# Performance work log

Hardware: AMD Instinct MI355X
Metric: run time of the kernel (lower is better)

## Reference

```python
import jax, jax.numpy as jnp
import numpy as np

B, T, E, D, H, DK, DV, C, FILT = 32, 2048, 1024, 1024, 4, 512, 512, 10, 100
K = 2 * FILT + 1  # conv kernel width = 201
SCALING = 2.0     # default forward scaling arg


def setup_inputs() -> dict:
    key = jax.random.key(0)
    ks = jax.random.split(key, 12)
    s = 0.02
    enc_hs_pad = jax.random.normal(ks[0], (B, T, E), dtype=jnp.float32)
    enc_hs_len = jax.random.randint(ks[1], (B,), T // 2, T + 1).astype(jnp.int32)
    dec_z = jax.random.normal(ks[2], (B, D), dtype=jnp.float32)
    # default att_prev in the module: uniform over valid frames (per head)
    valid = (jnp.arange(T)[None, :] < enc_hs_len[:, None]).astype(jnp.float32)  # (B,T)
    att_prev = jnp.broadcast_to((valid / enc_hs_len[:, None].astype(jnp.float32))[:, None, :], (B, H, T))
    return {
        "enc_hs_pad": enc_hs_pad,
        "enc_hs_len": enc_hs_len,
        "dec_z": dec_z,
        "att_prev": att_prev,
        "Wq": s * jax.random.normal(ks[3], (H, D, DK), dtype=jnp.float32),
        "bq": s * jax.random.normal(ks[4], (H, DK), dtype=jnp.float32),
        "Wk": s * jax.random.normal(ks[5], (H, E, DK), dtype=jnp.float32),
        "Wv": s * jax.random.normal(ks[6], (H, E, DV), dtype=jnp.float32),
        "gw": s * jax.random.normal(ks[7], (H, DK), dtype=jnp.float32),
        "gb": s * jax.random.normal(ks[8], (H,), dtype=jnp.float32),
        "conv_w": s * jax.random.normal(ks[9], (H, C, K), dtype=jnp.float32),
        "Watt": s * jax.random.normal(ks[10], (H, C, DK), dtype=jnp.float32),
        "Wo": s * jax.random.normal(ks[11], (H * DV, E), dtype=jnp.float32),
    }


def reference(enc_hs_pad, enc_hs_len, dec_z, att_prev, Wq, bq, Wk, Wv, gw, gb, conv_w, Watt, Wo):
    b, t, _ = enc_hs_pad.shape
    h, c_ch, kw = conv_w.shape
    # per-head key/value precomputes (vectorized over heads)
    k = jnp.einsum('bte,hek->bhtk', enc_hs_pad, Wk)          # (B,H,T,DK)
    v = jnp.einsum('bte,hev->bhtv', enc_hs_pad, Wv)          # (B,H,T,DV)
    q = jnp.einsum('bd,hdk->bhk', dec_z, Wq) + bq[None]      # (B,H,DK)
    # location conv: grouped 1D conv over T, one group per head
    conv_out = jax.lax.conv_general_dilated(
        att_prev,                                   # (B, H, T)
        conv_w.reshape(h * c_ch, 1, kw),            # (H*C, 1, K)
        window_strides=(1,),
        padding=[(FILT, FILT)],
        feature_group_count=h,
        dimension_numbers=('NCH', 'OIH', 'NCH'),
    ).reshape(b, h, c_ch, t)                        # (B,H,C,T)
    loc = jnp.einsum('bhct,hck->bhtk', conv_out, Watt)       # (B,H,T,DK)
    # additive score: gvec(tanh(k + loc + q))
    e = jnp.einsum('bhtk,hk->bht', jnp.tanh(k + loc + q[:, :, None, :]), gw) + gb[None, :, None]
    pad_mask = jnp.arange(t)[None, :] >= enc_hs_len[:, None]  # (B,T) True at pads
    e = jnp.where(pad_mask[:, None, :], -jnp.inf, e)
    w = jax.nn.softmax(SCALING * e, axis=-1)                 # (B,H,T)
    c = jnp.einsum('bhtv,bht->bhv', v, w).reshape(b, h * v.shape[-1]) @ Wo  # (B,E)
    return c, w
```

## Files before the change

kernel.cpp:

```cpp
#include <hip/hip_runtime.h>
#include <math.h>

#define B_ 32
#define T_ 2048
#define E_ 1024
#define D_ 1024
#define H_ 4
#define DK_ 512
#define DV_ 512
#define C_ 10
#define FILT_ 100
#define KW_ 201
#define SCALING_ 2.0f
#define KEXT_ 32

typedef __bf16 bf16_t;
typedef __bf16 bf16x8 __attribute__((ext_vector_type(8)));
typedef float f32x4 __attribute__((ext_vector_type(4)));

__device__ __forceinline__ float fast_tanh(float x) {
    x = fminf(15.f, fmaxf(-15.f, x));
    float e = __expf(2.f * x);
    return (e - 1.f) / (e + 1.f);
}

__device__ __forceinline__ void gload16(const void* g, void* l) {
  __builtin_amdgcn_global_load_lds(
      (const __attribute__((address_space(1))) void*)g,
      (__attribute__((address_space(3))) void*)l, 16, 0, 0);
}

__global__ __launch_bounds__(256) void tobf16_kernel(
    const float* __restrict__ in, bf16_t* __restrict__ out) {
  size_t i = ((size_t)blockIdx.x * 256 + threadIdx.x) * 8;
  float4 a = *(const float4*)(in + i);
  float4 b = *(const float4*)(in + i + 4);
  bf16x8 o;
  o[0] = (bf16_t)a.x; o[1] = (bf16_t)a.y; o[2] = (bf16_t)a.z; o[3] = (bf16_t)a.w;
  o[4] = (bf16_t)b.x; o[5] = (bf16_t)b.y; o[6] = (bf16_t)b.z; o[7] = (bf16_t)b.w;
  *(bf16x8*)(out + i) = o;
}

__global__ __launch_bounds__(256) void wkt_kernel(
    const float* __restrict__ Wk, bf16_t* __restrict__ WkT) {
  __shared__ float t[32][33];
  int h = blockIdx.z;
  int dk0 = blockIdx.x * 32, e0 = blockIdx.y * 32;
  int x = threadIdx.x & 31, y0 = threadIdx.x >> 5;
  for (int yy = 0; yy < 32; yy += 8) {
    int y = y0 + yy;
    t[y][x] = Wk[((size_t)h * E_ + e0 + y) * DK_ + dk0 + x];
  }
  __syncthreads();
  for (int yy = 0; yy < 32; yy += 8) {
    int y = y0 + yy;
    WkT[((size_t)h * DK_ + dk0 + y) * E_ + e0 + x] = (bf16_t)t[x][y];
  }
}

__global__ __launch_bounds__(256) void qproj_kernel(
    const float* __restrict__ dec_z, const float* __restrict__ Wq,
    const float* __restrict__ bq, float* __restrict__ q) {
  int idx = blockIdx.x * 256 + threadIdx.x;
  int dk = idx & (DK_ - 1);
  int h  = (idx >> 9) & (H_ - 1);
  int b  = idx >> 11;
  const float* dz = dec_z + (size_t)b * D_;
  const float* w  = Wq + (size_t)h * D_ * DK_ + dk;
  float s = bq[h * DK_ + dk];
  for (int d = 0; d < D_; ++d) s += dz[d] * w[(size_t)d * DK_];
  q[idx] = s;
}

__global__ __launch_bounds__(256) void cwt_kernel(
    const float* __restrict__ cw, float* __restrict__ cwT) {
  int idx = blockIdx.x * 256 + threadIdx.x;
  if (idx < H_ * C_ * KW_) {
    int k = idx % KW_;
    int c = (idx / KW_) % C_;
    int h = idx / (KW_ * C_);
    cwT[((size_t)h * KW_ + k) * C_ + c] = cw[idx];
  }
}

__global__ __launch_bounds__(256) void conv_kernel(
    const float* __restrict__ att_prev, const float* __restrict__ cwT,
    bf16_t* __restrict__ convT) {
  int bh = blockIdx.y;
  int h  = bh & (H_ - 1);
  int t0 = blockIdx.x * 256;
  int tid = threadIdx.x;
  __shared__ float sh[256 + 2 * FILT_];
  const float* ap = att_prev + (size_t)bh * T_;
  for (int f = tid; f < 256 + 2 * FILT_; f += 256) {
    int t = t0 + f - FILT_;
    sh[f] = (t >= 0 && t < T_) ? ap[t] : 0.f;
  }
  __syncthreads();
  const float* wt = cwT + (size_t)h * KW_ * C_;
  float out[C_];
#pragma unroll
  for (int c = 0; c < C_; ++c) out[c] = 0.f;
  for (int k = 0; k < KW_; ++k) {
    float x = sh[tid + k];
    const float* wk = wt + k * C_;
#pragma unroll
    for (int c = 0; c < C_; ++c) out[c] += wk[c] * x;
  }
  bf16_t* o = convT + ((size_t)bh * T_ + t0 + tid) * KEXT_;
#pragma unroll
  for (int c = 0; c < C_; ++c) o[c] = (bf16_t)out[c];
  o[C_] = (bf16_t)1.0f;
#pragma unroll
  for (int c = C_ + 1; c < KEXT_; ++c) o[c] = (bf16_t)0.0f;
}

__global__ __launch_bounds__(256) void bext_kernel(
    const float* __restrict__ Watt, const float* __restrict__ q,
    bf16_t* __restrict__ Bext) {
  int idx = blockIdx.x * 256 + threadIdx.x;
  int dk = idx & (DK_ - 1);
  int h = (idx >> 9) & (H_ - 1);
  bf16_t* o = Bext + (size_t)idx * KEXT_;
#pragma unroll
  for (int c = 0; c < C_; ++c) o[c] = (bf16_t)Watt[((size_t)h * C_ + c) * DK_ + dk];
  o[C_] = (bf16_t)q[idx];
#pragma unroll
  for (int c = C_ + 1; c < KEXT_; ++c) o[c] = (bf16_t)0.0f;
}

#define WT 128
#define WN 128
#define WKB 64
__global__ __launch_bounds__(256) void e_mfma_kernel(
    const bf16_t* __restrict__ encb, const bf16_t* __restrict__ WkT,
    const bf16_t* __restrict__ convT, const bf16_t* __restrict__ Bext,
    const float* __restrict__ gw, float* __restrict__ e_out) {
  __shared__ bf16_t As[WT * WKB];
  __shared__ bf16_t Bs[WN * WKB];
  int tid = threadIdx.x;
  int wave = tid >> 6, lane = tid & 63;
  int bh = blockIdx.z;
  int b = bh >> 2, h = bh & 3;
  int t0 = blockIdx.y * WT;
  int n0b = blockIdx.x * WN;
  const bf16_t* Ag = encb + ((size_t)b * T_ + t0) * E_;
  const bf16_t* Bg = WkT + ((size_t)h * DK_ + n0b) * E_;

  f32x4 acc[4][4] = {};

  int m0 = (wave & 1) * 64, n0 = (wave >> 1) * 64;
  int lr = lane & 15, lk = (lane >> 4) * 8;
  int srow = wave * 32 + (lane >> 3);
  int scol = (lane & 7) * 8;

  for (int e0 = 0; e0 < E_; e0 += WKB) {
#pragma unroll
    for (int j = 0; j < 4; ++j) {
      int r = srow + j * 8;
      gload16(Ag + (size_t)r * E_ + e0 + scol, As + r * WKB + scol);
      gload16(Bg + (size_t)r * E_ + e0 + scol, Bs + r * WKB + scol);
    }
    __syncthreads();
#pragma unroll
    for (int kk = 0; kk < WKB; kk += 32) {
      bf16x8 af[4], bfv[4];
#pragma unroll
      for (int i = 0; i < 4; ++i) {
        af[i]  = *(const bf16x8*)(As + (m0 + i * 16 + lr) * WKB + kk + lk);
        bfv[i] = *(const bf16x8*)(Bs + (n0 + i * 16 + lr) * WKB + kk + lk);
      }
#pragma unroll
      for (int i = 0; i < 4; ++i)
#pragma unroll
        for (int j = 0; j < 4; ++j)
          acc[i][j] = __builtin_amdgcn_mfma_f32_16x16x32_bf16(
              af[i], bfv[j], acc[i][j], 0, 0, 0);
    }
    __syncthreads();
  }

  {
    const bf16_t* Ag2 = convT + ((size_t)bh * T_ + t0) * KEXT_;
    const bf16_t* Bg2 = Bext + ((size_t)bh * DK_ + n0b) * KEXT_;
    int srow2 = wave * 32 + (lane >> 2);
    int scol2 = (lane & 3) * 8;
#pragma unroll
    for (int j = 0; j < 2; ++j) {
      int r = srow2 + j * 16;
      gload16(Ag2 + (size_t)r * KEXT_ + scol2, As + r * KEXT_ + scol2);
      gload16(Bg2 + (size_t)r * KEXT_ + scol2, Bs + r * KEXT_ + scol2);
    }
    __syncthreads();
    bf16x8 af[4], bfv[4];
#pragma unroll
    for (int i = 0; i < 4; ++i) {
      af[i]  = *(const bf16x8*)(As + (m0 + i * 16 + lr) * KEXT_ + lk);
      bfv[i] = *(const bf16x8*)(Bs + (n0 + i * 16 + lr) * KEXT_ + lk);
    }
#pragma unroll
    for (int i = 0; i < 4; ++i)
#pragma unroll
      for (int j = 0; j < 4; ++j)
        acc[i][j] = __builtin_amdgcn_mfma_f32_16x16x32_bf16(
            af[i], bfv[j], acc[i][j], 0, 0, 0);
  }

  float gwv[4];
#pragma unroll
  for (int j = 0; j < 4; ++j)
    gwv[j] = gw[(size_t)h * DK_ + n0b + n0 + j * 16 + lr];
  int rquad = (lane >> 4) * 4;
#pragma unroll
  for (int i = 0; i < 4; ++i) {
#pragma unroll
    for (int r = 0; r < 4; ++r) {
      int row = m0 + i * 16 + rquad + r;
      float part = 0.f;
#pragma unroll
      for (int j = 0; j < 4; ++j)
        part += fast_tanh(acc[i][j][r]) * gwv[j];
#pragma unroll
      for (int off = 8; off > 0; off >>= 1) part += __shfl_xor(part, off, 64);
      if (lr == 0) atomicAdd(e_out + (size_t)bh * T_ + t0 + row, part);
    }
  }
}

__global__ __launch_bounds__(256) void softmax_kernel(
    const float* __restrict__ e, const float* __restrict__ gb,
    const int* __restrict__ len, float* __restrict__ w_out) {
  int bh = blockIdx.x;
  int b = bh >> 2, h = bh & 3;
  int tid = threadIdx.x;
  int L = len[b];
  const float* er = e + (size_t)bh * T_;
  float* wr = w_out + (size_t)bh * T_;
  float gbh = gb[h];
  __shared__ float redA[4], redB[4];
  float mx = -1e30f;
  for (int t = tid; t < T_; t += 256)
    if (t < L) mx = fmaxf(mx, er[t] + gbh);
#pragma unroll
  for (int off = 32; off > 0; off >>= 1) mx = fmaxf(mx, __shfl_xor(mx, off, 64));
  if ((tid & 63) == 0) redA[tid >> 6] = mx;
  __syncthreads();
  mx = fmaxf(fmaxf(redA[0], redA[1]), fmaxf(redA[2], redA[3]));
  float sum = 0.f;
  for (int t = tid; t < T_; t += 256)
    if (t < L) sum += __expf(SCALING_ * ((er[t] + gbh) - mx));
#pragma unroll
  for (int off = 32; off > 0; off >>= 1) sum += __shfl_xor(sum, off, 64);
  if ((tid & 63) == 0) redB[tid >> 6] = sum;
  __syncthreads();
  sum = redB[0] + redB[1] + redB[2] + redB[3];
  float inv = 1.f / sum;
  for (int t = tid; t < T_; t += 256)
    wr[t] = (t < L) ? __expf(SCALING_ * ((er[t] + gbh) - mx)) * inv : 0.f;
}

#define TCH 256
__global__ __launch_bounds__(256) void wenc_kernel(
    const float* __restrict__ enc, const float* __restrict__ w,
    const int* __restrict__ len, float* __restrict__ we) {
  int b = blockIdx.y;
  int t0 = blockIdx.x * TCH;
  int L = len[b];
  if (t0 >= L) return;
  int tid = threadIdx.x;
  __shared__ float wS[H_ * TCH];
  const float* wb = w + (size_t)b * H_ * T_;
#pragma unroll
  for (int l = 0; l < H_; ++l)
    wS[l * TCH + tid] = wb[(size_t)l * T_ + t0 + tid];
  __syncthreads();
  const float4* encb = (const float4*)(enc + (size_t)b * T_ * E_);
  int tmax = min(TCH, L - t0);
  float4 a0 = {0.f, 0.f, 0.f, 0.f}, a1 = a0, a2 = a0, a3 = a0;
  for (int tt = 0; tt < tmax; ++tt) {
    float4 x = encb[(size_t)(t0 + tt) * (E_ / 4) + tid];
    float w0 = wS[tt], w1 = wS[TCH + tt], w2 = wS[2 * TCH + tt], w3 = wS[3 * TCH + tt];
    a0.x += w0 * x.x; a0.y += w0 * x.y; a0.z += w0 * x.z; a0.w += w0 * x.w;
    a1.x += w1 * x.x; a1.y += w1 * x.y; a1.z += w1 * x.z; a1.w += w1 * x.w;
    a2.x += w2 * x.x; a2.y += w2 * x.y; a2.z += w2 * x.z; a2.w += w2 * x.w;
    a3.x += w3 * x.x; a3.y += w3 * x.y; a3.z += w3 * x.z; a3.w += w3 * x.w;
  }
  float* p = we + (size_t)b * H_ * E_ + tid * 4;
  atomicAdd(p + 0 * E_ + 0, a0.x); atomicAdd(p + 0 * E_ + 1, a0.y);
  atomicAdd(p + 0 * E_ + 2, a0.z); atomicAdd(p + 0 * E_ + 3, a0.w);
  atomicAdd(p + 1 * E_ + 0, a1.x); atomicAdd(p + 1 * E_ + 1, a1.y);
  atomicAdd(p + 1 * E_ + 2, a1.z); atomicAdd(p + 1 * E_ + 3, a1.w);
  atomicAdd(p + 2 * E_ + 0, a2.x); atomicAdd(p + 2 * E_ + 1, a2.y);
  atomicAdd(p + 2 * E_ + 2, a2.z); atomicAdd(p + 2 * E_ + 3, a2.w);
  atomicAdd(p + 3 * E_ + 0, a3.x); atomicAdd(p + 3 * E_ + 1, a3.y);
  atomicAdd(p + 3 * E_ + 2, a3.z); atomicAdd(p + 3 * E_ + 3, a3.w);
}

__global__ __launch_bounds__(256) void ctx_kernel(
    const float* __restrict__ we, const float* __restrict__ Wv,
    float* __restrict__ ctx) {
  int idx = blockIdx.x * 256 + threadIdx.x;
  int dv = idx & (DV_ - 1);
  int bh = idx >> 9;
  int h = bh & 3;
  const float* weh = we + (size_t)bh * E_;
  const float* wvp = Wv + (size_t)h * E_ * DV_ + dv;
  float s = 0.f;
  for (int e = 0; e < E_; ++e) s += weh[e] * wvp[(size_t)e * DV_];
  ctx[idx] = s;
}

__global__ __launch_bounds__(256) void out_kernel(
    const float* __restrict__ ctx, const float* __restrict__ Wo,
    float* __restrict__ c_out) {
  int eo = blockIdx.x * 256 + threadIdx.x;
  int b = blockIdx.y;
  const float* cb = ctx + (size_t)b * (H_ * DV_);
  const float* wp = Wo + eo;
  float s = 0.f;
  for (int i = 0; i < H_ * DV_; ++i) s += cb[i] * wp[(size_t)i * E_];
  c_out[(size_t)b * E_ + eo] = s;
}

extern "C" void kernel_launch(void* const* d_in, const int* in_sizes, int n_in,
                              void* d_out, int out_size, void* d_ws, size_t ws_size,
                              hipStream_t stream) {
  const float* enc  = (const float*)d_in[0];
  const int*   len  = (const int*)d_in[1];
  const float* decz = (const float*)d_in[2];
  const float* attp = (const float*)d_in[3];
  const float* Wq   = (const float*)d_in[4];
  const float* bq   = (const float*)d_in[5];
  const float* Wk   = (const float*)d_in[6];
  const float* Wv   = (const float*)d_in[7];
  const float* gw   = (const float*)d_in[8];
  const float* gb   = (const float*)d_in[9];
  const float* cw   = (const float*)d_in[10];
  const float* Watt = (const float*)d_in[11];
  const float* Wo   = (const float*)d_in[12];

  float* c_out = (float*)d_out;
  float* w_out = c_out + (size_t)B_ * E_;

  float* q    = (float*)d_ws;
  float* e    = q   + (size_t)B_ * H_ * DK_;
  float* we   = e   + (size_t)B_ * H_ * T_;
  float* ctx  = we  + (size_t)B_ * H_ * E_;
  float* cwT  = ctx + (size_t)B_ * H_ * DV_;
  bf16_t* encb16 = (bf16_t*)(cwT + (size_t)H_ * KW_ * C_ + 64);
  bf16_t* WkT    = encb16 + (size_t)B_ * T_ * E_;
  bf16_t* convT  = WkT + (size_t)H_ * DK_ * E_;
  bf16_t* Bext   = convT + (size_t)B_ * H_ * T_ * KEXT_;

  hipMemsetAsync(e, 0, (size_t)B_ * H_ * T_ * sizeof(float), stream);
  hipMemsetAsync(we, 0, (size_t)B_ * H_ * E_ * sizeof(float), stream);

  tobf16_kernel<<<(size_t)B_ * T_ * E_ / 8 / 256, 256, 0, stream>>>(enc, encb16);
  wkt_kernel<<<dim3(DK_ / 32, E_ / 32, H_), 256, 0, stream>>>(Wk, WkT);
  qproj_kernel<<<B_ * H_ * DK_ / 256, 256, 0, stream>>>(decz, Wq, bq, q);
  cwt_kernel<<<(H_ * C_ * KW_ + 255) / 256, 256, 0, stream>>>(cw, cwT);
  conv_kernel<<<dim3(T_ / 256, B_ * H_), 256, 0, stream>>>(attp, cwT, convT);
  bext_kernel<<<B_ * H_ * DK_ / 256, 256, 0, stream>>>(Watt, q, Bext);
  e_mfma_kernel<<<dim3(DK_ / WN, T_ / WT, B_ * H_), 256, 0, stream>>>(
      encb16, WkT, convT, Bext, gw, e);
  softmax_kernel<<<B_ * H_, 256, 0, stream>>>(e, gb, len, w_out);
  wenc_kernel<<<dim3(T_ / TCH, B_), 256, 0, stream>>>(enc, w_out, len, we);
  ctx_kernel<<<B_ * H_ * DV_ / 256, 256, 0, stream>>>(we, Wv, ctx);
  out_kernel<<<dim3(E_ / 256, B_), 256, 0, stream>>>(ctx, Wo, c_out);
}
```

Before: 1.235 ms.

## Split-K the small projection GEMVs with atomics and swizzle MFMA LDS tiles

```diff
diff --git a/kernel.cpp b/kernel.cpp
--- a/kernel.cpp
+++ b/kernel.cpp
@@ -58,18 +58,21 @@
   }
 }
 
+#define QSPLIT 8
 __global__ __launch_bounds__(256) void qproj_kernel(
     const float* __restrict__ dec_z, const float* __restrict__ Wq,
     const float* __restrict__ bq, float* __restrict__ q) {
   int idx = blockIdx.x * 256 + threadIdx.x;
+  int s = blockIdx.y;
   int dk = idx & (DK_ - 1);
   int h  = (idx >> 9) & (H_ - 1);
   int b  = idx >> 11;
-  const float* dz = dec_z + (size_t)b * D_;
-  const float* w  = Wq + (size_t)h * D_ * DK_ + dk;
-  float s = bq[h * DK_ + dk];
-  for (int d = 0; d < D_; ++d) s += dz[d] * w[(size_t)d * DK_];
-  q[idx] = s;
+  const int CH = D_ / QSPLIT;
+  const float* dz = dec_z + (size_t)b * D_ + s * CH;
+  const float* w  = Wq + (size_t)h * D_ * DK_ + (size_t)(s * CH) * DK_ + dk;
+  float acc = (s == 0) ? bq[h * DK_ + dk] : 0.f;
+  for (int d = 0; d < CH; ++d) acc += dz[d] * w[(size_t)d * DK_];
+  atomicAdd(q + idx, acc);
 }
 
 __global__ __launch_bounds__(256) void cwt_kernel(
@@ -152,23 +155,25 @@
   int m0 = (wave & 1) * 64, n0 = (wave >> 1) * 64;
   int lr = lane & 15, lk = (lane >> 4) * 8;
   int srow = wave * 32 + (lane >> 3);
-  int scol = (lane & 7) * 8;
+  int cb   = lane & 7;
 
   for (int e0 = 0; e0 < E_; e0 += WKB) {
 #pragma unroll
     for (int j = 0; j < 4; ++j) {
       int r = srow + j * 8;
-      gload16(Ag + (size_t)r * E_ + e0 + scol, As + r * WKB + scol);
-      gload16(Bg + (size_t)r * E_ + e0 + scol, Bs + r * WKB + scol);
+      int gc = (cb ^ (r & 7)) * 8;
+      gload16(Ag + (size_t)r * E_ + e0 + gc, As + r * WKB + cb * 8);
+      gload16(Bg + (size_t)r * E_ + e0 + gc, Bs + r * WKB + cb * 8);
     }
     __syncthreads();
 #pragma unroll
     for (int kk = 0; kk < WKB; kk += 32) {
+      int sc = ((((kk + lk) >> 3) ^ (lr & 7)) << 3);
       bf16x8 af[4], bfv[4];
 #pragma unroll
       for (int i = 0; i < 4; ++i) {
-        af[i]  = *(const bf16x8*)(As + (m0 + i * 16 + lr) * WKB + kk + lk);
-        bfv[i] = *(const bf16x8*)(Bs + (n0 + i * 16 + lr) * WKB + kk + lk);
+        af[i]  = *(const bf16x8*)(As + (m0 + i * 16 + lr) * WKB + sc);
+        bfv[i] = *(const bf16x8*)(Bs + (n0 + i * 16 + lr) * WKB + sc);
       }
 #pragma unroll
       for (int i = 0; i < 4; ++i)
@@ -296,30 +301,36 @@
   atomicAdd(p + 3 * E_ + 2, a3.z); atomicAdd(p + 3 * E_ + 3, a3.w);
 }
 
+#define CSPLIT 8
 __global__ __launch_bounds__(256) void ctx_kernel(
     const float* __restrict__ we, const float* __restrict__ Wv,
     float* __restrict__ ctx) {
   int idx = blockIdx.x * 256 + threadIdx.x;
+  int s = blockIdx.y;
   int dv = idx & (DV_ - 1);
   int bh = idx >> 9;
   int h = bh & 3;
-  const float* weh = we + (size_t)bh * E_;
-  const float* wvp = Wv + (size_t)h * E_ * DV_ + dv;
-  float s = 0.f;
-  for (int e = 0; e < E_; ++e) s += weh[e] * wvp[(size_t)e * DV_];
-  ctx[idx] = s;
-}
-
+  const int CH = E_ / CSPLIT;
+  const float* weh = we + (size_t)bh * E_ + s * CH;
+  const float* wvp = Wv + (size_t)h * E_ * DV_ + (size_t)(s * CH) * DV_ + dv;
+  float acc = 0.f;
+  for (int e = 0; e < CH; ++e) acc += weh[e] * wvp[(size_t)e * DV_];
+  atomicAdd(ctx + idx, acc);
+}
+
+#define OSPLIT 8
 __global__ __launch_bounds__(256) void out_kernel(
     const float* __restrict__ ctx, const float* __restrict__ Wo,
     float* __restrict__ c_out) {
   int eo = blockIdx.x * 256 + threadIdx.x;
   int b = blockIdx.y;
-  const float* cb = ctx + (size_t)b * (H_ * DV_);
-  const float* wp = Wo + eo;
-  float s = 0.f;
-  for (int i = 0; i < H_ * DV_; ++i) s += cb[i] * wp[(size_t)i * E_];
-  c_out[(size_t)b * E_ + eo] = s;
+  int s = blockIdx.z;
+  const int CH = (H_ * DV_) / OSPLIT;
+  const float* cb = ctx + (size_t)b * (H_ * DV_) + s * CH;
+  const float* wp = Wo + (size_t)(s * CH) * E_ + eo;
+  float acc = 0.f;
+  for (int i = 0; i < CH; ++i) acc += cb[i] * wp[(size_t)i * E_];
+  atomicAdd(c_out + (size_t)b * E_ + eo, acc);
 }
 
 extern "C" void kernel_launch(void* const* d_in, const int* in_sizes, int n_in,
@@ -352,12 +363,15 @@
   bf16_t* convT  = WkT + (size_t)H_ * DK_ * E_;
   bf16_t* Bext   = convT + (size_t)B_ * H_ * T_ * KEXT_;
 
+  hipMemsetAsync(q, 0, (size_t)B_ * H_ * DK_ * sizeof(float), stream);
   hipMemsetAsync(e, 0, (size_t)B_ * H_ * T_ * sizeof(float), stream);
   hipMemsetAsync(we, 0, (size_t)B_ * H_ * E_ * sizeof(float), stream);
+  hipMemsetAsync(ctx, 0, (size_t)B_ * H_ * DV_ * sizeof(float), stream);
+  hipMemsetAsync(c_out, 0, (size_t)B_ * E_ * sizeof(float), stream);
 
   tobf16_kernel<<<(size_t)B_ * T_ * E_ / 8 / 256, 256, 0, stream>>>(enc, encb16);
   wkt_kernel<<<dim3(DK_ / 32, E_ / 32, H_), 256, 0, stream>>>(Wk, WkT);
-  qproj_kernel<<<B_ * H_ * DK_ / 256, 256, 0, stream>>>(decz, Wq, bq, q);
+  qproj_kernel<<<dim3(B_ * H_ * DK_ / 256, QSPLIT), 256, 0, stream>>>(decz, Wq, bq, q);
   cwt_kernel<<<(H_ * C_ * KW_ + 255) / 256, 256, 0, stream>>>(cw, cwT);
   conv_kernel<<<dim3(T_ / 256, B_ * H_), 256, 0, stream>>>(attp, cwT, convT);
   bext_kernel<<<B_ * H_ * DK_ / 256, 256, 0, stream>>>(Watt, q, Bext);
@@ -365,6 +379,6 @@
       encb16, WkT, convT, Bext, gw, e);
   softmax_kernel<<<B_ * H_, 256, 0, stream>>>(e, gb, len, w_out);
   wenc_kernel<<<dim3(T_ / TCH, B_), 256, 0, stream>>>(enc, w_out, len, we);
-  ctx_kernel<<<B_ * H_ * DV_ / 256, 256, 0, stream>>>(we, Wv, ctx);
-  out_kernel<<<dim3(E_ / 256, B_), 256, 0, stream>>>(ctx, Wo, c_out);
-}
+  ctx_kernel<<<dim3(B_ * H_ * DV_ / 256, CSPLIT), 256, 0, stream>>>(we, Wv, ctx);
+  out_kernel<<<dim3(E_ / 256, B_, OSPLIT), 256, 0, stream>>>(ctx, Wo, c_out);
+}
```

Measured after the change: 1.108 ms. -10.3%, faster.
